# Kernel tuning notes

Measured on AMD Instinct MI355X. Metric: run time of the kernel, lower is better.

The kernel has to match this reference:

```python
import jax, jax.numpy as jnp
import numpy as np

DECAY = 0.8
EPS = 1e-05


def setup_inputs() -> dict:
    key = jax.random.key(0)
    k1, k2, k3 = jax.random.split(key, 3)
    b, n, d = 16, 4096, 64
    h, c = 1, 2048
    x = jax.random.normal(k1, (b, n, d), dtype=jnp.float32)
    embeddings = jax.random.normal(k2, (h, c, d), dtype=jnp.float32)
    cluster_size = jnp.ones((h, c), dtype=jnp.float32)
    embed_avg = jax.random.normal(k3, (h, c, d), dtype=jnp.float32)
    return {"x": x, "embeddings": embeddings, "cluster_size": cluster_size, "embed_avg": embed_avg}


def reference(x, embeddings, cluster_size, embed_avg):
    # x: (b, n, d); add codebook dim h=1 and flatten -> (h, N, d)
    d = x.shape[-1]
    flat = x.reshape(1, -1, d)                              # (h, N, d)
    h, C = embeddings.shape[0], embeddings.shape[1]

    # dist = -cdist(flat, embeddings)  (negative euclidean distance)
    x2 = jnp.sum(flat * flat, axis=-1, keepdims=True)       # (h, N, 1)
    e2 = jnp.sum(embeddings * embeddings, axis=-1)          # (h, C)
    xe = jnp.einsum('hnd,hcd->hnc', flat, embeddings)       # (h, N, C)
    dist = -jnp.sqrt(jnp.clip(x2 + e2[:, None, :] - 2.0 * xe, 0.0))

    # gumbel_sample with stochastic=False, straight_through=False -> hard argmax
    embed_ind = jnp.argmax(dist, axis=-1)                   # (h, N)

    # quantize: gather selected codes
    quantize = jnp.take_along_axis(embeddings, embed_ind[..., None], axis=1)  # (h, N, d)

    # EMA codebook update (scatter-based): counts and per-code feature sums
    counts = jax.vmap(lambda i: jnp.bincount(i, length=C))(embed_ind).astype(x.dtype)  # (h, C)
    embed_sum = jax.vmap(lambda f, i: jax.ops.segment_sum(f, i, num_segments=C))(flat, embed_ind)  # (h, C, d)

    new_cluster_size = cluster_size * DECAY + counts * (1.0 - DECAY)
    new_embed_avg = embed_avg * DECAY + embed_sum * (1.0 - DECAY)

    # laplace smoothing of cluster sizes, then renormalize embed_avg
    tot = jnp.sum(new_cluster_size, axis=-1, keepdims=True)
    smoothed = (new_cluster_size + EPS) / (tot + C * EPS) * tot
    new_embeddings = new_embed_avg / smoothed[..., None]

    quantize = quantize.reshape(x.shape)                    # drop h dim back to (b, n, d)
    embed_ind = embed_ind.reshape(x.shape[:-1])             # (b, n)
    return quantize, embed_ind, new_embeddings, new_cluster_size, new_embed_avg
```

## Files before the change

### kernel.cpp

```cpp
#include <hip/hip_runtime.h>

#define N_TOK 65536
#define D 64
#define C_CODES 2048
#define DECAYF 0.8f
#define OMDF 0.2f
#define EPSF 1e-5f
#define SEG 16
#define KSLOT 30
#define CAND_MAX 8
#define MARGIN 0.125f
#define TCODES 32
#define NT (C_CODES / TCODES)
#define NSUB (C_CODES / 16)

#define OUT_QUANT 0
#define OUT_IND   (N_TOK * D)
#define OUT_EMB   (OUT_IND + N_TOK)
#define OUT_CS    (OUT_EMB + C_CODES * D)
#define OUT_EAVG  (OUT_CS + C_CODES)

typedef short s16x8 __attribute__((ext_vector_type(8)));
typedef float f32x4 __attribute__((ext_vector_type(4)));

__device__ __forceinline__ unsigned short f2bf(float f) {
    unsigned int u = __float_as_uint(f);
    return (unsigned short)((u + 0x7fffu + ((u >> 16) & 1u)) >> 16);
}
__device__ __forceinline__ float bf2f(unsigned short h) {
    return __uint_as_float(((unsigned int)h) << 16);
}
__device__ __forceinline__ unsigned long long shflx64(unsigned long long v, int mask) {
    unsigned int lo = (unsigned int)v, hi = (unsigned int)(v >> 32);
    lo = __shfl_xor(lo, mask, 64);
    hi = __shfl_xor(hi, mask, 64);
    return ((unsigned long long)hi << 32) | lo;
}
__device__ __forceinline__ void gload_lds16(const void* g, void* l) {
    __builtin_amdgcn_global_load_lds(
        (const __attribute__((address_space(1))) void*)g,
        (__attribute__((address_space(3))) void*)l, 16, 0, 0);
}

__global__ void e2_kernel(const float* __restrict__ emb, float* __restrict__ e2) {
    int c = blockIdx.x * blockDim.x + threadIdx.x;
    const float4* er = (const float4*)(emb + (size_t)c * D);
    float s0 = 0.f, s1 = 0.f, s2 = 0.f, s3 = 0.f;
#pragma unroll
    for (int i = 0; i < D / 4; ++i) {
        float4 e = er[i];
        s0 = fmaf(e.x, e.x, s0);
        s1 = fmaf(e.y, e.y, s1);
        s2 = fmaf(e.z, e.z, s2);
        s3 = fmaf(e.w, e.w, s3);
    }
    e2[c] = (s0 + s1) + (s2 + s3);
}

__global__ void eprep_kernel(const float* __restrict__ emb, short* __restrict__ ebk,
                             float* __restrict__ counts, float* __restrict__ embed_sum) {
    int g = blockIdx.x * blockDim.x + threadIdx.x;
    int code = g >> 3, slot = g & 7;
    int kc = slot ^ (code & 7);
    const float4* ep = (const float4*)(emb + (size_t)code * D + kc * 8);
    float4 a = ep[0], b = ep[1];
    float v[8] = {a.x, a.y, a.z, a.w, b.x, b.y, b.z, b.w};
    s16x8 h, l;
#pragma unroll
    for (int j = 0; j < 8; ++j) {
        unsigned short hb = f2bf(v[j]);
        h[j] = (short)hb;
        l[j] = (short)f2bf(v[j] - bf2f(hb));
    }
    *(s16x8*)(ebk + (size_t)code * 128 + slot * 8) = h;
    *(s16x8*)(ebk + (size_t)code * 128 + 64 + slot * 8) = l;

    float4 z = {0.f, 0.f, 0.f, 0.f};
    ((float4*)embed_sum)[g * 2] = z;
    ((float4*)embed_sum)[g * 2 + 1] = z;
    if (g < C_CODES / 4) ((float4*)counts)[g] = z;
}

__device__ __forceinline__ void cand_insert(int t, int code, float score,
                                            int* cnt, int* ccode, float* cscore) {
    int slot = atomicAdd(&cnt[t], 1);
    if (slot < KSLOT) {
        ccode[t * KSLOT + slot] = code;
        cscore[t * KSLOT + slot] = score;
    }
}

__global__ __launch_bounds__(256) void screen_kernel(
        const float* __restrict__ x, const short* __restrict__ ebk,
        const float* __restrict__ e2, int* __restrict__ gcount,
        int* __restrict__ gcand) {
    __shared__ float e2s[C_CODES];
    __shared__ __align__(16) char bstage[2][TCODES * 256];
    __shared__ int cnt[64];
    __shared__ float finmin[64];
    __shared__ int ccode[64 * KSLOT];
    __shared__ float cscore[64 * KSLOT];

    const int tid = threadIdx.x;
    ((float4*)e2s)[tid] = ((const float4*)e2)[tid];
    ((float4*)e2s)[tid + 256] = ((const float4*)e2)[tid + 256];
    if (tid < 64) cnt[tid] = 0;

    const int lane = tid & 63;
    const int wave = tid >> 6;
    const int col = lane & 15;
    const int krow = lane >> 4;
    const int atok = blockIdx.x * 64 + wave * 16 + col;
    const int tokbase = wave * 16 + krow * 4;

    const float4* xp = (const float4*)(x + (size_t)atok * D + krow * 8);
    float4 f0 = xp[0], f1 = xp[1], f2 = xp[8], f3 = xp[9];
    float xv[16] = {f0.x, f0.y, f0.z, f0.w, f1.x, f1.y, f1.z, f1.w,
                    f2.x, f2.y, f2.z, f2.w, f3.x, f3.y, f3.z, f3.w};
    s16x8 ah0, ah1, al0, al1;
#pragma unroll
    for (int j = 0; j < 8; ++j) {
        unsigned short h0 = f2bf(xv[j]);
        ah0[j] = (short)h0;
        al0[j] = (short)f2bf(xv[j] - bf2f(h0));
        unsigned short h1 = f2bf(xv[8 + j]);
        ah1[j] = (short)h1;
        al1[j] = (short)f2bf(xv[8 + j] - bf2f(h1));
    }

    auto stage = [&](int b, int t) {
        const char* src = (const char*)ebk + (size_t)t * (TCODES * 256)
                          + wave * 2048 + lane * 16;
        char* dst = &bstage[b][wave * 2048];
        gload_lds16(src, dst);
        gload_lds16(src + 1024, dst + 1024);
    };

    auto subtile = [&](const char* lb, int st, float* sc_) {
        const char* base = lb + ((st & 1) << 12) + (col << 8);
        int off = (krow ^ (col & 7)) << 4;
        s16x8 bh0 = *(const s16x8*)(base + off);
        s16x8 bh1 = *(const s16x8*)(base + (off ^ 64));
        s16x8 bl0 = *(const s16x8*)(base + 128 + off);
        s16x8 bl1 = *(const s16x8*)(base + 128 + (off ^ 64));
        f32x4 a0 = {0.f, 0.f, 0.f, 0.f};
        f32x4 a1 = {0.f, 0.f, 0.f, 0.f};
        f32x4 a2 = {0.f, 0.f, 0.f, 0.f};
        a0 = __builtin_amdgcn_mfma_f32_16x16x32_bf16(ah0, bh0, a0, 0, 0, 0);
        a1 = __builtin_amdgcn_mfma_f32_16x16x32_bf16(al0, bh0, a1, 0, 0, 0);
        a2 = __builtin_amdgcn_mfma_f32_16x16x32_bf16(ah0, bl0, a2, 0, 0, 0);
        a0 = __builtin_amdgcn_mfma_f32_16x16x32_bf16(ah1, bh1, a0, 0, 0, 0);
        a1 = __builtin_amdgcn_mfma_f32_16x16x32_bf16(al1, bh1, a1, 0, 0, 0);
        a2 = __builtin_amdgcn_mfma_f32_16x16x32_bf16(ah1, bl1, a2, 0, 0, 0);
        float e2c = e2s[st * 16 + col];
#pragma unroll
        for (int r = 0; r < 4; ++r)
            sc_[r] = fmaf(-2.0f, (a0[r] + a1[r]) + a2[r], e2c);
    };

    float rmin[4], sc[4];

    auto normal = [&](int st) {
        int codeb = st * 16 + col;
#pragma unroll
        for (int r = 0; r < 4; ++r) {
            if (sc[r] <= rmin[r] + MARGIN)
                cand_insert(tokbase + r, codeb, sc[r], cnt, ccode, cscore);
            rmin[r] = fminf(rmin[r], sc[r]);
        }
        int mk = 1 << (st & 3);
#pragma unroll
        for (int r = 0; r < 4; ++r)
            rmin[r] = fminf(rmin[r], __shfl_xor(rmin[r], mk, 16));
    };

    stage(0, 0);
    __syncthreads();

    stage(1, 1);
    subtile(bstage[0], 0, sc);
#pragma unroll
    for (int r = 0; r < 4; ++r) rmin[r] = sc[r];
#pragma unroll
    for (int mk = 1; mk < 16; mk <<= 1)
#pragma unroll
        for (int r = 0; r < 4; ++r)
            rmin[r] = fminf(rmin[r], __shfl_xor(rmin[r], mk, 16));
#pragma unroll
    for (int r = 0; r < 4; ++r)
        if (sc[r] <= rmin[r] + MARGIN)
            cand_insert(tokbase + r, col, sc[r], cnt, ccode, cscore);
    subtile(bstage[0], 1, sc);
    normal(1);
    __syncthreads();

    for (int t = 1; t < NT; ++t) {
        if (t + 1 < NT) stage((t + 1) & 1, t + 1);
        const char* lb = bstage[t & 1];
        subtile(lb, 2 * t, sc);
        normal(2 * t);
        subtile(lb, 2 * t + 1, sc);
        normal(2 * t + 1);
        __syncthreads();
    }

#pragma unroll
    for (int mk = 1; mk < 16; mk <<= 1)
#pragma unroll
        for (int r = 0; r < 4; ++r)
            rmin[r] = fminf(rmin[r], __shfl_xor(rmin[r], mk, 16));
    if (col == 0) {
#pragma unroll
        for (int r = 0; r < 4; ++r) finmin[tokbase + r] = rmin[r];
    }
    __syncthreads();

    if (tid < 64) {
        int t = tid;
        int gt = blockIdx.x * 64 + t;
        int m = cnt[t];
        int om = 0;
        if (m > KSLOT) {
            om = 255;
        } else {
            float thr = finmin[t] + MARGIN;
            for (int i = 0; i < m; ++i) {
                if (cscore[t * KSLOT + i] <= thr) {
                    if (om < CAND_MAX) gcand[gt * CAND_MAX + om] = ccode[t * KSLOT + i];
                    om++;
                }
            }
            if (om > CAND_MAX) om = 255;
        }
        gcount[gt] = om;
    }
}

__global__ __launch_bounds__(256) void exact_kernel(
        const float* __restrict__ x, const float* __restrict__ emb,
        const float* __restrict__ e2,
        const int* __restrict__ gcount, const int* __restrict__ gcand,
        int* __restrict__ idx, float* __restrict__ out,
        float* __restrict__ counts) {
    __shared__ float lcount[C_CODES];
    for (int i = threadIdx.x; i < C_CODES; i += blockDim.x) lcount[i] = 0.0f;
    __syncthreads();
    int n = blockIdx.x * blockDim.x + threadIdx.x;
    int lane = threadIdx.x & 63;

    const float4* xr = (const float4*)(x + (size_t)n * D);
    float4 xv[D / 4];
#pragma unroll
    for (int i = 0; i < D / 4; ++i) xv[i] = xr[i];
    float s0 = 0.f, s1 = 0.f, s2 = 0.f, s3 = 0.f;
#pragma unroll
    for (int i = 0; i < D / 4; ++i) {
        s0 = fmaf(xv[i].x, xv[i].x, s0);
        s1 = fmaf(xv[i].y, xv[i].y, s1);
        s2 = fmaf(xv[i].z, xv[i].z, s2);
        s3 = fmaf(xv[i].w, xv[i].w, s3);
    }
    float x2 = (s0 + s1) + (s2 + s3);

    unsigned long long best = ~0ull;
    int m = gcount[n];
    bool fb = (m < 1 || m > CAND_MAX);
    if (!fb) {
        for (int i = 0; i < m; ++i) {
            int c = gcand[n * CAND_MAX + i];
            const float4* er = (const float4*)(emb + (size_t)c * D);
            float d0 = 0.f, d1 = 0.f, d2 = 0.f, d3 = 0.f;
#pragma unroll
            for (int i2 = 0; i2 < D / 4; ++i2) {
                float4 e = er[i2];
                d0 = fmaf(xv[i2].x, e.x, d0);
                d1 = fmaf(xv[i2].y, e.y, d1);
                d2 = fmaf(xv[i2].z, e.z, d2);
                d3 = fmaf(xv[i2].w, e.w, d3);
            }
            float dot = (d0 + d1) + (d2 + d3);
            float dist2 = x2 + e2[c] - 2.0f * dot;
            dist2 = fmaxf(dist2, 0.0f);
            unsigned long long key =
                ((unsigned long long)__float_as_uint(dist2) << 32) | (unsigned int)c;
            best = key < best ? key : best;
        }
    }

    unsigned long long bal = __ballot(fb);
    while (bal) {
        int src = (int)__ffsll((long long)bal) - 1;
        bal &= bal - 1;
        int tn = (n & ~63) + src;
        const float4* tr = (const float4*)(x + (size_t)tn * D);
        float4 tv[D / 4];
#pragma unroll
        for (int i = 0; i < D / 4; ++i) tv[i] = tr[i];
        float t0 = 0.f, t1 = 0.f, t2 = 0.f, t3 = 0.f;
#pragma unroll
        for (int i = 0; i < D / 4; ++i) {
            t0 = fmaf(tv[i].x, tv[i].x, t0);
            t1 = fmaf(tv[i].y, tv[i].y, t1);
            t2 = fmaf(tv[i].z, tv[i].z, t2);
            t3 = fmaf(tv[i].w, tv[i].w, t3);
        }
        float tx2 = (t0 + t1) + (t2 + t3);
        unsigned long long kbest = ~0ull;
        for (int c = lane; c < C_CODES; c += 64) {
            const float4* er = (const float4*)(emb + (size_t)c * D);
            float d0 = 0.f, d1 = 0.f, d2 = 0.f, d3 = 0.f;
#pragma unroll
            for (int i = 0; i < D / 4; ++i) {
                float4 e = er[i];
                d0 = fmaf(tv[i].x, e.x, d0);
                d1 = fmaf(tv[i].y, e.y, d1);
                d2 = fmaf(tv[i].z, e.z, d2);
                d3 = fmaf(tv[i].w, e.w, d3);
            }
            float dot = (d0 + d1) + (d2 + d3);
            float dist2 = tx2 + e2[c] - 2.0f * dot;
            dist2 = fmaxf(dist2, 0.0f);
            unsigned long long key =
                ((unsigned long long)__float_as_uint(dist2) << 32) | (unsigned int)c;
            kbest = key < kbest ? key : kbest;
        }
#pragma unroll
        for (int mk = 1; mk < 64; mk <<= 1) {
            unsigned long long o = shflx64(kbest, mk);
            kbest = o < kbest ? o : kbest;
        }
        if (lane == src) best = kbest;
    }

    int c = (int)(best & 0xffffffffull);
    idx[n] = c;
    out[OUT_IND + n] = (float)c;
    atomicAdd(&lcount[c], 1.0f);
    __syncthreads();
    for (int i = threadIdx.x; i < C_CODES; i += blockDim.x) {
        float v = lcount[i];
        if (v != 0.0f) atomicAdd(&counts[i], v);
    }
}

__global__ void gather_kernel(const float* __restrict__ emb,
                              const int* __restrict__ idx,
                              float* __restrict__ out) {
    int g = blockIdx.x * blockDim.x + threadIdx.x;
    int n = g >> 4;
    int j = g & 15;
    int c = idx[n];
    float4 e = ((const float4*)emb)[c * (D / 4) + j];
    ((float4*)(out + OUT_QUANT))[g] = e;
}

__global__ void prefix_ema_kernel(const float* __restrict__ counts,
                                  const float* __restrict__ cluster_size,
                                  float* __restrict__ out,
                                  float* __restrict__ smoothed,
                                  int* __restrict__ cursor) {
    __shared__ float scan[256];
    __shared__ float red[256];
    int t = threadIdx.x;
    int base = t * 8;
    float cnt[8], ncs[8];
    float csum = 0.f, nsum = 0.f;
#pragma unroll
    for (int j = 0; j < 8; ++j) {
        cnt[j] = counts[base + j];
        csum += cnt[j];
        ncs[j] = cluster_size[base + j] * DECAYF + cnt[j] * OMDF;
        nsum += ncs[j];
        out[OUT_CS + base + j] = ncs[j];
    }
    scan[t] = csum;
    red[t] = nsum;
    __syncthreads();
    for (int s = 1; s < 256; s <<= 1) {
        float v = scan[t];
        float w = (t >= s) ? scan[t - s] : 0.f;
        __syncthreads();
        scan[t] = v + w;
        __syncthreads();
    }
    for (int s = 128; s > 0; s >>= 1) {
        if (t < s) red[t] += red[t + s];
        __syncthreads();
    }
    float tot = red[0];
    float run = (t == 0) ? 0.f : scan[t - 1];
#pragma unroll
    for (int j = 0; j < 8; ++j) {
        cursor[base + j] = (int)run;
        run += cnt[j];
        smoothed[base + j] = (ncs[j] + EPSF) / (tot + (float)C_CODES * EPSF) * tot;
    }
}

__global__ void scatter_pos_kernel(const int* __restrict__ idx,
                                   int* __restrict__ cursor,
                                   unsigned int* __restrict__ sorted) {
    int n = blockIdx.x * blockDim.x + threadIdx.x;
    int c = idx[n];
    int pos = atomicAdd(&cursor[c], 1);
    sorted[pos] = ((unsigned int)c << 16) | (unsigned int)n;
}

__global__ __launch_bounds__(256) void seg_sum_kernel(
        const float* __restrict__ x, const unsigned int* __restrict__ sorted,
        float* __restrict__ embed_sum) {
    int lane = threadIdx.x & 63;
    int q = blockIdx.x * 4 + (threadIdx.x >> 6);
    int p0 = q * SEG;

    unsigned int mine = (lane < SEG) ? sorted[p0 + lane] : 0u;
    unsigned int pk[SEG];
#pragma unroll
    for (int j = 0; j < SEG; ++j) pk[j] = __shfl(mine, j, 64);

    float xv[SEG];
#pragma unroll
    for (int j = 0; j < SEG; ++j)
        xv[j] = x[(size_t)(pk[j] & 0xffffu) * D + lane];

    unsigned int run_c = 0xffffffffu;
    float sum = 0.f;
#pragma unroll
    for (int j = 0; j < SEG; ++j) {
        unsigned int c = pk[j] >> 16;
        if (c != run_c) {
            if (run_c != 0xffffffffu)
                atomicAdd(&embed_sum[(size_t)run_c * D + lane], sum);
            run_c = c;
            sum = 0.f;
        }
        sum += xv[j];
    }
    atomicAdd(&embed_sum[(size_t)run_c * D + lane], sum);
}

__global__ void ema_embed_kernel(const float* __restrict__ embed_avg,
                                 const float* __restrict__ embed_sum,
                                 const float* __restrict__ smoothed,
                                 float* __restrict__ out) {
    int g = blockIdx.x * blockDim.x + threadIdx.x;
    int c = g >> 4;
    float4 ea = ((const float4*)embed_avg)[g];
    float4 es = ((const float4*)embed_sum)[g];
    float4 na;
    na.x = ea.x * DECAYF + es.x * OMDF;
    na.y = ea.y * DECAYF + es.y * OMDF;
    na.z = ea.z * DECAYF + es.z * OMDF;
    na.w = ea.w * DECAYF + es.w * OMDF;
    ((float4*)(out + OUT_EAVG))[g] = na;
    float sm = smoothed[c];
    float4 ne;
    ne.x = na.x / sm;
    ne.y = na.y / sm;
    ne.z = na.z / sm;
    ne.w = na.w / sm;
    ((float4*)(out + OUT_EMB))[g] = ne;
}

extern "C" void kernel_launch(void* const* d_in, const int* in_sizes, int n_in,
                              void* d_out, int out_size, void* d_ws, size_t ws_size,
                              hipStream_t stream) {
    const float* x            = (const float*)d_in[0];
    const float* emb          = (const float*)d_in[1];
    const float* cluster_size = (const float*)d_in[2];
    const float* embed_avg    = (const float*)d_in[3];
    float* out = (float*)d_out;

    float* e2        = (float*)d_ws;
    float* counts    = e2 + C_CODES;
    float* smoothed  = counts + C_CODES;
    int*   cursor    = (int*)(smoothed + C_CODES);
    int*   idx       = cursor + C_CODES;
    unsigned int* sorted = (unsigned int*)(idx + N_TOK);
    int*   gcount    = (int*)(sorted + N_TOK);
    int*   gcand     = gcount + N_TOK;
    float* embed_sum = (float*)(gcand + (size_t)N_TOK * CAND_MAX);
    short* ebk       = (short*)(embed_sum + C_CODES * D);

    e2_kernel<<<C_CODES / 256, 256, 0, stream>>>(emb, e2);
    eprep_kernel<<<(C_CODES * 8) / 256, 256, 0, stream>>>(emb, ebk, counts, embed_sum);
    screen_kernel<<<N_TOK / 64, 256, 0, stream>>>(x, ebk, e2, gcount, gcand);
    exact_kernel<<<N_TOK / 256, 256, 0, stream>>>(x, emb, e2, gcount, gcand, idx, out, counts);
    gather_kernel<<<(N_TOK * 16) / 256, 256, 0, stream>>>(emb, idx, out);
    prefix_ema_kernel<<<1, 256, 0, stream>>>(counts, cluster_size, out, smoothed, cursor);
    scatter_pos_kernel<<<N_TOK / 256, 256, 0, stream>>>(idx, cursor, sorted);
    seg_sum_kernel<<<(N_TOK / SEG) / 4, 256, 0, stream>>>(x, sorted, embed_sum);
    ema_embed_kernel<<<(C_CODES * 16) / 256, 256, 0, stream>>>(embed_avg, embed_sum,
                                                              smoothed, out);
}
```

Measured before the change: 278.5 us.

## Track top-2 scores in screening and skip exact recheck unless gap is small

The screening kernel now keeps each token's best and second-best approximate scores and best code in registers, replacing the LDS candidate lists and atomics. e2 is folded into the MFMA accumulation via a ones-vector trick, and -2 is folded into x. Each block covers 128 tokens so every staged codebook tile is reused twice. Tokens whose top-2 gap exceeds a threshold take the screened code directly; the rest fall back to a full exact scan. This removes the exact-candidate FP32 pass for most tokens, but correctness now depends on the split-bf16 precision staying within the gap threshold.

Result: slower. 381.0 us (+36.8%).

```diff
diff --git a/kernel.cpp b/kernel.cpp
--- a/kernel.cpp
+++ b/kernel.cpp
@@ -7,12 +7,9 @@
 #define OMDF 0.2f
 #define EPSF 1e-5f
 #define SEG 16
-#define KSLOT 30
-#define CAND_MAX 8
-#define MARGIN 0.125f
+#define GAP_THR 0.03125f
 #define TCODES 32
 #define NT (C_CODES / TCODES)
-#define NSUB (C_CODES / 16)
 
 #define OUT_QUANT 0
 #define OUT_IND   (N_TOK * D)
@@ -42,7 +39,8 @@
         (__attribute__((address_space(3))) void*)l, 16, 0, 0);
 }
 
-__global__ void e2_kernel(const float* __restrict__ emb, float* __restrict__ e2) {
+__global__ void e2_kernel(const float* __restrict__ emb, float* __restrict__ e2,
+                          unsigned int* __restrict__ e2p) {
     int c = blockIdx.x * blockDim.x + threadIdx.x;
     const float4* er = (const float4*)(emb + (size_t)c * D);
     float s0 = 0.f, s1 = 0.f, s2 = 0.f, s3 = 0.f;
@@ -54,7 +52,11 @@
         s2 = fmaf(e.z, e.z, s2);
         s3 = fmaf(e.w, e.w, s3);
     }
-    e2[c] = (s0 + s1) + (s2 + s3);
+    float v = (s0 + s1) + (s2 + s3);
+    e2[c] = v;
+    unsigned short hb = f2bf(v);
+    unsigned short lb = f2bf(v - bf2f(hb));
+    e2p[c] = (unsigned int)hb | ((unsigned int)lb << 16);
 }
 
 __global__ void eprep_kernel(const float* __restrict__ emb, short* __restrict__ ebk,
@@ -81,52 +83,60 @@
     if (g < C_CODES / 4) ((float4*)counts)[g] = z;
 }
 
-__device__ __forceinline__ void cand_insert(int t, int code, float score,
-                                            int* cnt, int* ccode, float* cscore) {
-    int slot = atomicAdd(&cnt[t], 1);
-    if (slot < KSLOT) {
-        ccode[t * KSLOT + slot] = code;
-        cscore[t * KSLOT + slot] = score;
-    }
-}
-
 __global__ __launch_bounds__(256) void screen_kernel(
         const float* __restrict__ x, const short* __restrict__ ebk,
-        const float* __restrict__ e2, int* __restrict__ gcount,
-        int* __restrict__ gcand) {
-    __shared__ float e2s[C_CODES];
+        const unsigned int* __restrict__ e2p, unsigned int* __restrict__ gbest) {
+    __shared__ unsigned int e2pl[C_CODES];
     __shared__ __align__(16) char bstage[2][TCODES * 256];
-    __shared__ int cnt[64];
-    __shared__ float finmin[64];
-    __shared__ int ccode[64 * KSLOT];
-    __shared__ float cscore[64 * KSLOT];
 
     const int tid = threadIdx.x;
-    ((float4*)e2s)[tid] = ((const float4*)e2)[tid];
-    ((float4*)e2s)[tid + 256] = ((const float4*)e2)[tid + 256];
-    if (tid < 64) cnt[tid] = 0;
+    ((uint4*)e2pl)[tid] = ((const uint4*)e2p)[tid];
+    ((uint4*)e2pl)[tid + 256] = ((const uint4*)e2p)[tid + 256];
 
     const int lane = tid & 63;
     const int wave = tid >> 6;
     const int col = lane & 15;
     const int krow = lane >> 4;
-    const int atok = blockIdx.x * 64 + wave * 16 + col;
-    const int tokbase = wave * 16 + krow * 4;
-
-    const float4* xp = (const float4*)(x + (size_t)atok * D + krow * 8);
-    float4 f0 = xp[0], f1 = xp[1], f2 = xp[8], f3 = xp[9];
-    float xv[16] = {f0.x, f0.y, f0.z, f0.w, f1.x, f1.y, f1.z, f1.w,
-                    f2.x, f2.y, f2.z, f2.w, f3.x, f3.y, f3.z, f3.w};
-    s16x8 ah0, ah1, al0, al1;
-#pragma unroll
-    for (int j = 0; j < 8; ++j) {
-        unsigned short h0 = f2bf(xv[j]);
-        ah0[j] = (short)h0;
-        al0[j] = (short)f2bf(xv[j] - bf2f(h0));
-        unsigned short h1 = f2bf(xv[8 + j]);
-        ah1[j] = (short)h1;
-        al1[j] = (short)f2bf(xv[8 + j] - bf2f(h1));
-    }
+
+    s16x8 ah[2][2], al[2][2];
+#pragma unroll
+    for (int s = 0; s < 2; ++s) {
+        int tok = blockIdx.x * 128 + wave * 32 + s * 16 + col;
+        const float4* xp = (const float4*)(x + (size_t)tok * D + krow * 8);
+        float4 f0 = xp[0], f1 = xp[1], f2 = xp[8], f3 = xp[9];
+        float xv[16] = {f0.x, f0.y, f0.z, f0.w, f1.x, f1.y, f1.z, f1.w,
+                        f2.x, f2.y, f2.z, f2.w, f3.x, f3.y, f3.z, f3.w};
+#pragma unroll
+        for (int j = 0; j < 8; ++j) {
+            float v0 = -2.0f * xv[j];
+            unsigned short h0 = f2bf(v0);
+            ah[s][0][j] = (short)h0;
+            al[s][0][j] = (short)f2bf(v0 - bf2f(h0));
+            float v1 = -2.0f * xv[8 + j];
+            unsigned short h1 = f2bf(v1);
+            ah[s][1][j] = (short)h1;
+            al[s][1][j] = (short)f2bf(v1 - bf2f(h1));
+        }
+    }
+
+    s16x8 aone = {0, 0, 0, 0, 0, 0, 0, 0};
+    {
+        short o = (krow == 0) ? (short)0x3F80 : (short)0;
+        aone[0] = o;
+        aone[1] = o;
+    }
+    const f32x4 zero = {0.f, 0.f, 0.f, 0.f};
+
+    float b1[2][4], b2[2][4];
+    unsigned int bc[2][4];
+#pragma unroll
+    for (int s = 0; s < 2; ++s)
+#pragma unroll
+        for (int r = 0; r < 4; ++r) {
+            b1[s][r] = __builtin_inff();
+            b2[s][r] = __builtin_inff();
+            bc[s][r] = 0u;
+        }
 
     auto stage = [&](int b, int t) {
         const char* src = (const char*)ebk + (size_t)t * (TCODES * 256)
@@ -136,110 +146,75 @@
         gload_lds16(src + 1024, dst + 1024);
     };
 
-    auto subtile = [&](const char* lb, int st, float* sc_) {
+    auto subtile = [&](const char* lb, int st) {
         const char* base = lb + ((st & 1) << 12) + (col << 8);
         int off = (krow ^ (col & 7)) << 4;
         s16x8 bh0 = *(const s16x8*)(base + off);
         s16x8 bh1 = *(const s16x8*)(base + (off ^ 64));
         s16x8 bl0 = *(const s16x8*)(base + 128 + off);
         s16x8 bl1 = *(const s16x8*)(base + 128 + (off ^ 64));
-        f32x4 a0 = {0.f, 0.f, 0.f, 0.f};
-        f32x4 a1 = {0.f, 0.f, 0.f, 0.f};
-        f32x4 a2 = {0.f, 0.f, 0.f, 0.f};
-        a0 = __builtin_amdgcn_mfma_f32_16x16x32_bf16(ah0, bh0, a0, 0, 0, 0);
-        a1 = __builtin_amdgcn_mfma_f32_16x16x32_bf16(al0, bh0, a1, 0, 0, 0);
-        a2 = __builtin_amdgcn_mfma_f32_16x16x32_bf16(ah0, bl0, a2, 0, 0, 0);
-        a0 = __builtin_amdgcn_mfma_f32_16x16x32_bf16(ah1, bh1, a0, 0, 0, 0);
-        a1 = __builtin_amdgcn_mfma_f32_16x16x32_bf16(al1, bh1, a1, 0, 0, 0);
-        a2 = __builtin_amdgcn_mfma_f32_16x16x32_bf16(ah1, bl1, a2, 0, 0, 0);
-        float e2c = e2s[st * 16 + col];
-#pragma unroll
-        for (int r = 0; r < 4; ++r)
-            sc_[r] = fmaf(-2.0f, (a0[r] + a1[r]) + a2[r], e2c);
-    };
-
-    float rmin[4], sc[4];
-
-    auto normal = [&](int st) {
-        int codeb = st * 16 + col;
-#pragma unroll
-        for (int r = 0; r < 4; ++r) {
-            if (sc[r] <= rmin[r] + MARGIN)
-                cand_insert(tokbase + r, codeb, sc[r], cnt, ccode, cscore);
-            rmin[r] = fminf(rmin[r], sc[r]);
-        }
-        int mk = 1 << (st & 3);
-#pragma unroll
-        for (int r = 0; r < 4; ++r)
-            rmin[r] = fminf(rmin[r], __shfl_xor(rmin[r], mk, 16));
+        unsigned int code = (unsigned int)(st * 16 + col);
+        unsigned int v = e2pl[st * 16 + col];
+        v = (krow == 0) ? v : 0u;
+        s16x8 be2 = {(short)(v & 0xffffu), (short)(v >> 16), 0, 0, 0, 0, 0, 0};
+        f32x4 f = __builtin_amdgcn_mfma_f32_16x16x32_bf16(aone, be2, zero, 0, 0, 0);
+#pragma unroll
+        for (int s = 0; s < 2; ++s) {
+            f32x4 a0 = __builtin_amdgcn_mfma_f32_16x16x32_bf16(ah[s][1], bh1, f, 0, 0, 0);
+            a0 = __builtin_amdgcn_mfma_f32_16x16x32_bf16(ah[s][0], bh0, a0, 0, 0, 0);
+            f32x4 a1 = __builtin_amdgcn_mfma_f32_16x16x32_bf16(al[s][1], bh1, zero, 0, 0, 0);
+            a1 = __builtin_amdgcn_mfma_f32_16x16x32_bf16(al[s][0], bh0, a1, 0, 0, 0);
+            f32x4 a2 = __builtin_amdgcn_mfma_f32_16x16x32_bf16(ah[s][1], bl1, zero, 0, 0, 0);
+            a2 = __builtin_amdgcn_mfma_f32_16x16x32_bf16(ah[s][0], bl0, a2, 0, 0, 0);
+#pragma unroll
+            for (int r = 0; r < 4; ++r) {
+                float sc = (a0[r] + a1[r]) + a2[r];
+                bool take = sc < b1[s][r];
+                b2[s][r] = fminf(b2[s][r], fmaxf(sc, b1[s][r]));
+                b1[s][r] = fminf(b1[s][r], sc);
+                bc[s][r] = take ? code : bc[s][r];
+            }
+        }
     };
 
     stage(0, 0);
     __syncthreads();
 
-    stage(1, 1);
-    subtile(bstage[0], 0, sc);
-#pragma unroll
-    for (int r = 0; r < 4; ++r) rmin[r] = sc[r];
-#pragma unroll
-    for (int mk = 1; mk < 16; mk <<= 1)
-#pragma unroll
-        for (int r = 0; r < 4; ++r)
-            rmin[r] = fminf(rmin[r], __shfl_xor(rmin[r], mk, 16));
-#pragma unroll
-    for (int r = 0; r < 4; ++r)
-        if (sc[r] <= rmin[r] + MARGIN)
-            cand_insert(tokbase + r, col, sc[r], cnt, ccode, cscore);
-    subtile(bstage[0], 1, sc);
-    normal(1);
-    __syncthreads();
-
-    for (int t = 1; t < NT; ++t) {
+    for (int t = 0; t < NT; ++t) {
         if (t + 1 < NT) stage((t + 1) & 1, t + 1);
         const char* lb = bstage[t & 1];
-        subtile(lb, 2 * t, sc);
-        normal(2 * t);
-        subtile(lb, 2 * t + 1, sc);
-        normal(2 * t + 1);
+        subtile(lb, 2 * t);
+        subtile(lb, 2 * t + 1);
         __syncthreads();
     }
 
 #pragma unroll
-    for (int mk = 1; mk < 16; mk <<= 1)
-#pragma unroll
-        for (int r = 0; r < 4; ++r)
-            rmin[r] = fminf(rmin[r], __shfl_xor(rmin[r], mk, 16));
-    if (col == 0) {
-#pragma unroll
-        for (int r = 0; r < 4; ++r) finmin[tokbase + r] = rmin[r];
-    }
-    __syncthreads();
-
-    if (tid < 64) {
-        int t = tid;
-        int gt = blockIdx.x * 64 + t;
-        int m = cnt[t];
-        int om = 0;
-        if (m > KSLOT) {
-            om = 255;
-        } else {
-            float thr = finmin[t] + MARGIN;
-            for (int i = 0; i < m; ++i) {
-                if (cscore[t * KSLOT + i] <= thr) {
-                    if (om < CAND_MAX) gcand[gt * CAND_MAX + om] = ccode[t * KSLOT + i];
-                    om++;
-                }
+    for (int s = 0; s < 2; ++s)
+#pragma unroll
+        for (int r = 0; r < 4; ++r) {
+            float B1 = b1[s][r], B2 = b2[s][r];
+            unsigned int C1 = bc[s][r];
+#pragma unroll
+            for (int mk = 1; mk < 16; mk <<= 1) {
+                float o1 = __shfl_xor(B1, mk, 16);
+                float o2 = __shfl_xor(B2, mk, 16);
+                unsigned int oc = (unsigned int)__shfl_xor((int)C1, mk, 16);
+                float hi = fmaxf(B1, o1);
+                B2 = fminf(fminf(B2, o2), hi);
+                bool take = o1 < B1;
+                B1 = fminf(B1, o1);
+                C1 = take ? oc : C1;
             }
-            if (om > CAND_MAX) om = 255;
-        }
-        gcount[gt] = om;
-    }
+            if (col == 0) {
+                int gt = blockIdx.x * 128 + wave * 32 + s * 16 + krow * 4 + r;
+                gbest[gt] = ((B2 - B1 <= GAP_THR) ? 0x80000000u : 0u) | C1;
+            }
+        }
 }
 
 __global__ __launch_bounds__(256) void exact_kernel(
         const float* __restrict__ x, const float* __restrict__ emb,
-        const float* __restrict__ e2,
-        const int* __restrict__ gcount, const int* __restrict__ gcand,
+        const float* __restrict__ e2, const unsigned int* __restrict__ gbest,
         int* __restrict__ idx, float* __restrict__ out,
         float* __restrict__ counts) {
     __shared__ float lcount[C_CODES];
@@ -248,44 +223,9 @@
     int n = blockIdx.x * blockDim.x + threadIdx.x;
     int lane = threadIdx.x & 63;
 
-    const float4* xr = (const float4*)(x + (size_t)n * D);
-    float4 xv[D / 4];
-#pragma unroll
-    for (int i = 0; i < D / 4; ++i) xv[i] = xr[i];
-    float s0 = 0.f, s1 = 0.f, s2 = 0.f, s3 = 0.f;
-#pragma unroll
-    for (int i = 0; i < D / 4; ++i) {
-        s0 = fmaf(xv[i].x, xv[i].x, s0);
-        s1 = fmaf(xv[i].y, xv[i].y, s1);
-        s2 = fmaf(xv[i].z, xv[i].z, s2);
-        s3 = fmaf(xv[i].w, xv[i].w, s3);
-    }
-    float x2 = (s0 + s1) + (s2 + s3);
-
-    unsigned long long best = ~0ull;
-    int m = gcount[n];
-    bool fb = (m < 1 || m > CAND_MAX);
-    if (!fb) {
-        for (int i = 0; i < m; ++i) {
-            int c = gcand[n * CAND_MAX + i];
-            const float4* er = (const float4*)(emb + (size_t)c * D);
-            float d0 = 0.f, d1 = 0.f, d2 = 0.f, d3 = 0.f;
-#pragma unroll
-            for (int i2 = 0; i2 < D / 4; ++i2) {
-                float4 e = er[i2];
-                d0 = fmaf(xv[i2].x, e.x, d0);
-                d1 = fmaf(xv[i2].y, e.y, d1);
-                d2 = fmaf(xv[i2].z, e.z, d2);
-                d3 = fmaf(xv[i2].w, e.w, d3);
-            }
-            float dot = (d0 + d1) + (d2 + d3);
-            float dist2 = x2 + e2[c] - 2.0f * dot;
-            dist2 = fmaxf(dist2, 0.0f);
-            unsigned long long key =
-                ((unsigned long long)__float_as_uint(dist2) << 32) | (unsigned int)c;
-            best = key < best ? key : best;
-        }
-    }
+    unsigned int v = gbest[n];
+    int c = (int)(v & 0x7fffffffu);
+    bool fb = (v >> 31) != 0u;
 
     unsigned long long bal = __ballot(fb);
     while (bal) {
@@ -306,8 +246,8 @@
         }
         float tx2 = (t0 + t1) + (t2 + t3);
         unsigned long long kbest = ~0ull;
-        for (int c = lane; c < C_CODES; c += 64) {
-            const float4* er = (const float4*)(emb + (size_t)c * D);
+        for (int cc = lane; cc < C_CODES; cc += 64) {
+            const float4* er = (const float4*)(emb + (size_t)cc * D);
             float d0 = 0.f, d1 = 0.f, d2 = 0.f, d3 = 0.f;
 #pragma unroll
             for (int i = 0; i < D / 4; ++i) {
@@ -318,10 +258,10 @@
                 d3 = fmaf(tv[i].w, e.w, d3);
             }
             float dot = (d0 + d1) + (d2 + d3);
-            float dist2 = tx2 + e2[c] - 2.0f * dot;
+            float dist2 = tx2 + e2[cc] - 2.0f * dot;
             dist2 = fmaxf(dist2, 0.0f);
             unsigned long long key =
-                ((unsigned long long)__float_as_uint(dist2) << 32) | (unsigned int)c;
+                ((unsigned long long)__float_as_uint(dist2) << 32) | (unsigned int)cc;
             kbest = key < kbest ? key : kbest;
         }
 #pragma unroll
@@ -329,17 +269,16 @@
             unsigned long long o = shflx64(kbest, mk);
             kbest = o < kbest ? o : kbest;
         }
-        if (lane == src) best = kbest;
-    }
-
-    int c = (int)(best & 0xffffffffull);
+        if (lane == src) c = (int)(kbest & 0xffffffffull);
+    }
+
     idx[n] = c;
     out[OUT_IND + n] = (float)c;
     atomicAdd(&lcount[c], 1.0f);
     __syncthreads();
     for (int i = threadIdx.x; i < C_CODES; i += blockDim.x) {
-        float v = lcount[i];
-        if (v != 0.0f) atomicAdd(&counts[i], v);
+        float vv = lcount[i];
+        if (vv != 0.0f) atomicAdd(&counts[i], vv);
     }
 }
 
@@ -472,20 +411,20 @@
     float* out = (float*)d_out;
 
     float* e2        = (float*)d_ws;
-    float* counts    = e2 + C_CODES;
+    unsigned int* e2p = (unsigned int*)(e2 + C_CODES);
+    float* counts    = (float*)(e2p + C_CODES);
     float* smoothed  = counts + C_CODES;
     int*   cursor    = (int*)(smoothed + C_CODES);
     int*   idx       = cursor + C_CODES;
     unsigned int* sorted = (unsigned int*)(idx + N_TOK);
-    int*   gcount    = (int*)(sorted + N_TOK);
-    int*   gcand     = gcount + N_TOK;
-    float* embed_sum = (float*)(gcand + (size_t)N_TOK * CAND_MAX);
+    unsigned int* gbest  = sorted + N_TOK;
+    float* embed_sum = (float*)(gbest + N_TOK);
     short* ebk       = (short*)(embed_sum + C_CODES * D);
 
-    e2_kernel<<<C_CODES / 256, 256, 0, stream>>>(emb, e2);
+    e2_kernel<<<C_CODES / 256, 256, 0, stream>>>(emb, e2, e2p);
     eprep_kernel<<<(C_CODES * 8) / 256, 256, 0, stream>>>(emb, ebk, counts, embed_sum);
-    screen_kernel<<<N_TOK / 64, 256, 0, stream>>>(x, ebk, e2, gcount, gcand);
-    exact_kernel<<<N_TOK / 256, 256, 0, stream>>>(x, emb, e2, gcount, gcand, idx, out, counts);
+    screen_kernel<<<N_TOK / 128, 256, 0, stream>>>(x, ebk, e2p, gbest);
+    exact_kernel<<<N_TOK / 256, 256, 0, stream>>>(x, emb, e2, gbest, idx, out, counts);
     gather_kernel<<<(N_TOK * 16) / 256, 256, 0, stream>>>(emb, idx, out);
     prefix_ema_kernel<<<1, 256, 0, stream>>>(counts, cluster_size, out, smoothed, cursor);
     scatter_pos_kernel<<<N_TOK / 256, 256, 0, stream>>>(idx, cursor, sorted);
```
